# Optimization experiments

Hardware: AMD Instinct MI355X
Metric: run time of the kernel (lower is better)

## Reference

```python
import jax, jax.numpy as jnp
import numpy as np

PS, PAD, STRIDE = 3, 1, 1  # patch_size, padding, strides


def _unfold(x, ps, pad, stride):
    # torch F.unfold: [N, C, H, W] -> [N, C*ps*ps, L], channel-major (c, i, j) ordering
    N, C, H, Wd = x.shape
    xp = jnp.pad(x, ((0, 0), (0, 0), (pad, pad), (pad, pad)))
    Ho = (H + 2 * pad - ps) // stride + 1
    Wo = (Wd + 2 * pad - ps) // stride + 1
    cols = [xp[:, :, i:i + stride * Ho:stride, j:j + stride * Wo:stride]
            for i in range(ps) for j in range(ps)]  # ps*ps tensors of [N, C, Ho, Wo]
    cols = jnp.stack(cols, axis=2)                  # [N, C, ps*ps, Ho, Wo]
    return cols.reshape(N, C * ps * ps, Ho * Wo)


def _fold(cols, out_hw, ps, pad, stride):
    # torch F.fold (scatter-add inverse of unfold)
    N, CPP, L = cols.shape
    C = CPP // (ps * ps)
    H, Wd = out_hw
    Ho = (H + 2 * pad - ps) // stride + 1
    Wo = (Wd + 2 * pad - ps) // stride + 1
    cols = cols.reshape(N, C, ps, ps, Ho, Wo)
    out = jnp.zeros((N, C, H + 2 * pad, Wd + 2 * pad), cols.dtype)
    for i in range(ps):
        for j in range(ps):
            out = out.at[:, :, i:i + stride * Ho:stride, j:j + stride * Wo:stride].add(cols[:, :, i, j])
    return out[:, :, pad:pad + H, pad:pad + Wd]


def _l2norm(x, eps=1e-12):
    n = jnp.sqrt(jnp.sum(x * x, axis=-1, keepdims=True))
    return x / jnp.maximum(n, eps)


def setup_inputs() -> dict:
    key = jax.random.key(0)
    k1, k2, k3, k4 = jax.random.split(key, 4)
    shp = (2, 64, 5, 5, 48, 48)  # b, c, ah, aw, h, w
    return {
        "x1": jax.random.normal(k1, shp, dtype=jnp.float32),
        "x2": jax.random.normal(k2, shp, dtype=jnp.float32),
        "x3": jax.random.normal(k3, shp, dtype=jnp.float32),
        "W": jax.random.normal(k4, (8, 64), dtype=jnp.float32) * 0.05,  # 1x1 conv, c -> c//8
    }


def reference(x1, x2, x3, W):
    b, c, ah, aw, h, w = x1.shape
    A = ah * aw

    def flat(x):  # b c ah aw h w -> (b ah aw) c h w
        return x.transpose(0, 2, 3, 1, 4, 5).reshape(b * A, c, h, w)

    q = jnp.einsum('oc,nchw->nohw', W, flat(x1))  # 1x1 conv, no bias
    k = jnp.einsum('oc,nchw->nohw', W, flat(x2))
    v = flat(x3)

    qc = _unfold(q, PS, PAD, STRIDE)  # [(b ah aw), p_q, L]
    kc = _unfold(k, PS, PAD, STRIDE)
    vc = _unfold(v, PS, PAD, STRIDE)  # [(b ah aw), p_v, L]
    L = vc.shape[-1]
    p_v = vc.shape[1]

    def re(t):  # (b ah aw) p n -> b n (ah aw p)
        p = t.shape[1]
        return t.reshape(b, A, p, L).transpose(0, 3, 1, 2).reshape(b, L, A * p)

    Q = _l2norm(re(qc))
    K = _l2norm(re(kc))
    V = re(vc)  # [b, L, A*p_v]

    attn = jnp.einsum('bnd,bmd->bnm', Q, K)       # [b, L, L] cosine similarity
    idx = jnp.argmax(attn, axis=-1)               # [b, L] hard attention
    out = jnp.take_along_axis(V, idx[:, :, None], axis=1)  # gather rows of V

    # b n (ah aw p) -> (b ah aw) p n
    out = out.reshape(b, L, A, p_v).transpose(0, 2, 3, 1).reshape(b * A, p_v, L)
    out = _fold(out, (h, w), PS, PAD, STRIDE)     # [(b ah aw), c, h, w]
    return out.reshape(b, ah, aw, c, h, w).transpose(0, 3, 1, 2, 4, 5)
```

## Files before the change

### kernel.cpp

```cpp
#include <hip/hip_runtime.h>
#include <math.h>
#include <float.h>

#define NPIX 2304
#define NPAD 2500
#define PLANE 573440
#define MARGIN 3e-4f

#define OFF_QP     0u
#define OFF_KP     1146880u
#define OFF_PLANES 2293760u
#define OFF_TAIL   4587520u
#define OFF_NK     4751360u
#define OFF_INVNK  4756360u
#define OFF_PVAL   4760968u
#define OFF_PSEC   4982152u
#define OFF_PIDX   5203336u
#define OFF_IDX    5424520u
#define OFF_S      5429128u
#define OFF_SOFF   OFF_S
#define SSTRIDE    6250000L
#define PLANE_SH   573440

typedef __attribute__((ext_vector_type(8))) short short8;
typedef __attribute__((ext_vector_type(4))) float f32x4;

__device__ __forceinline__ unsigned short bfhi(float f) {
    unsigned u = __float_as_uint(f);
    return (unsigned short)((u + 0x7FFFu + ((u >> 16) & 1u)) >> 16);
}

__device__ __forceinline__ void gload_lds16(const void* g, void* l) {
    __builtin_amdgcn_global_load_lds(
        (const __attribute__((address_space(1))) unsigned int*)g,
        (__attribute__((address_space(3))) unsigned int*)l, 16, 0, 0);
}

__global__ __launch_bounds__(256) void k_zero(float4* __restrict__ p, int n4) {
    int i = blockIdx.x * 256 + threadIdx.x;
    const int stride = gridDim.x * 256;
    const float4 z = { 0.f, 0.f, 0.f, 0.f };
    for (; i < n4; i += stride) p[i] = z;
}

__global__ __launch_bounds__(256) void k_qk(const float* __restrict__ x1,
                                            const float* __restrict__ x2,
                                            const float* __restrict__ W,
                                            float* __restrict__ qp,
                                            float* __restrict__ kp,
                                            unsigned short* __restrict__ planes,
                                            unsigned short* __restrict__ tail) {
    __shared__ float Ws[512];
    const int t = threadIdx.x;
    Ws[t] = W[t];
    Ws[t + 256] = W[t + 256];
    __syncthreads();
    const int img = blockIdx.x / 9;
    const int chunk = blockIdx.x % 9;
    const int pix = chunk * 256 + t;
    const int b = img / 25, a = img % 25;
    const int y = pix / 48, x = pix % 48;

    float q[8], k[8];
#pragma unroll
    for (int o = 0; o < 8; ++o) { q[o] = 0.f; k[o] = 0.f; }

    const float* p1 = x1 + (size_t)b * 64 * 57600 + a * 2304 + pix;
    const float* p2 = x2 + (size_t)b * 64 * 57600 + a * 2304 + pix;
#pragma unroll 8
    for (int c = 0; c < 64; ++c) {
        float v1 = p1[c * 57600];
        float v2 = p2[c * 57600];
#pragma unroll
        for (int o = 0; o < 8; ++o) {
            float w = Ws[o * 64 + c];
            q[o] = fmaf(w, v1, q[o]);
            k[o] = fmaf(w, v2, k[o]);
        }
    }
    const int p = (y + 1) * 50 + (x + 1);
    float* qd = qp + (size_t)b * PLANE + (size_t)p * 224 + a * 8;
    float* kd = kp + (size_t)b * PLANE + (size_t)p * 224 + a * 8;
    float4 q0 = { q[0], q[1], q[2], q[3] }, q1 = { q[4], q[5], q[6], q[7] };
    float4 k0 = { k[0], k[1], k[2], k[3] }, k1 = { k[4], k[5], k[6], k[7] };
    *(float4*)qd = q0; *(float4*)(qd + 4) = q1;
    *(float4*)kd = k0; *(float4*)(kd + 4) = k1;

    const int P = p >> 7, r = p & 127, cc = a >> 2, dq = a & 3;
    const int g = r * 4 + ((dq + (r >> 1)) & 3);
    const size_t goff = ((size_t)(P * 7 + cc) * 512 + g) * 8;
    short8 qh, ql, kh, kl;
#pragma unroll
    for (int o = 0; o < 8; ++o) {
        unsigned short h = bfhi(q[o]);
        qh[o] = (short)h;
        ql[o] = (short)bfhi(q[o] - __uint_as_float(((unsigned)h) << 16));
        h = bfhi(k[o]);
        kh[o] = (short)h;
        kl[o] = (short)bfhi(k[o] - __uint_as_float(((unsigned)h) << 16));
    }
    *(short8*)(planes + (size_t)(0 * 2 + b) * PLANE_SH + goff) = qh;
    *(short8*)(planes + (size_t)(1 * 2 + b) * PLANE_SH + goff) = ql;
    *(short8*)(planes + (size_t)(2 * 2 + b) * PLANE_SH + goff) = kh;
    *(short8*)(planes + (size_t)(3 * 2 + b) * PLANE_SH + goff) = kl;

    if (a == 24) {
        unsigned short* qt = tail + (((size_t)(0 * 2 + b) * 20 + P) << 12);
        unsigned short* kt = tail + (((size_t)(1 * 2 + b) * 20 + P) << 12);
        short8 zz = { 0, 0, 0, 0, 0, 0, 0, 0 };
#define GOF(qq) ((r * 4 + (((qq) + (r >> 1)) & 3)) * 8)
        *(short8*)(qt + GOF(0)) = qh;
        *(short8*)(qt + GOF(1)) = qh;
        *(short8*)(qt + GOF(2)) = ql;
        *(short8*)(qt + GOF(3)) = zz;
        *(short8*)(kt + GOF(0)) = kh;
        *(short8*)(kt + GOF(1)) = kl;
        *(short8*)(kt + GOF(2)) = kh;
        *(short8*)(kt + GOF(3)) = zz;
#undef GOF
    }
}

__global__ void k_nk(const float* __restrict__ kp, float* __restrict__ nk) {
    int t = blockIdx.x * 256 + threadIdx.x;
    if (t >= 2 * NPAD) return;
    int b = t / NPAD, p = t - b * NPAD;
    const float* src = kp + (size_t)b * PLANE + (size_t)p * 224;
    float s = 0.f;
    for (int d = 0; d < 200; d += 4) {
        float4 v = *(const float4*)(src + d);
        s = fmaf(v.x, v.x, s); s = fmaf(v.y, v.y, s);
        s = fmaf(v.z, v.z, s); s = fmaf(v.w, v.w, s);
    }
    nk[t] = s;
}

__global__ void k_invnk(const float* __restrict__ nk, float* __restrict__ invNk) {
    int t = blockIdx.x * 256 + threadIdx.x;
    if (t >= 2 * NPIX) return;
    int b = t / NPIX, m = t - b * NPIX;
    int my = m / 48, mx = m % 48;
    const float* nb = nk + b * NPAD;
    float s = 0.f;
#pragma unroll
    for (int i = 0; i < 3; ++i)
#pragma unroll
        for (int j = 0; j < 3; ++j)
            s += nb[(my + i) * 50 + mx + j];
    invNk[t] = 1.0f / fmaxf(sqrtf(s), 1e-12f);
}

__global__ __launch_bounds__(256, 2) void k_mfma2(const unsigned short* __restrict__ planes,
                                                  const unsigned short* __restrict__ tail,
                                                  float* __restrict__ S,
                                                  long sStride, int bofs) {
    __shared__ unsigned short Abuf[2][4096];
    __shared__ unsigned short Bbuf[2][4096];
    const int t = threadIdx.x;
    const int nwg = gridDim.x * gridDim.y * gridDim.z;
    const int lin = (blockIdx.z * gridDim.y + blockIdx.y) * gridDim.x + blockIdx.x;
    const int work = (lin & 7) * (nwg >> 3) + (lin >> 3);
    const int z = work / 400;
    const int rem = work - z * 400;
    const int wy = rem / 20, wx = rem - (rem / 20) * 20;
    const int b = bofs + z;

    const unsigned short* Ahi = planes + (size_t)(0 * 2 + b) * PLANE_SH;
    const unsigned short* Alo = planes + (size_t)(1 * 2 + b) * PLANE_SH;
    const unsigned short* Bhi = planes + (size_t)(2 * 2 + b) * PLANE_SH;
    const unsigned short* Blo = planes + (size_t)(3 * 2 + b) * PLANE_SH;
    float* Sb = S + (size_t)z * sStride;

    const int p0 = wy * 128, r0 = wx * 128;
    const int wid = t >> 6, l = t & 63;
    const int lp = l & 15, dq = l >> 4;
    const int wqp = (wid >> 1) * 64, wqr = (wid & 1) * 64;

    int aoff[4], boff[4];
#pragma unroll
    for (int tr = 0; tr < 4; ++tr) {
        int rA = wqp + tr * 16 + lp;
        aoff[tr] = (rA * 4 + ((dq + (rA >> 1)) & 3)) * 8;
        int rB = wqr + tr * 16 + lp;
        boff[tr] = (rB * 4 + ((dq + (rB >> 1)) & 3)) * 8;
    }

    f32x4 acc[4][4];
#pragma unroll
    for (int i = 0; i < 4; ++i)
#pragma unroll
        for (int j = 0; j < 4; ++j) acc[i][j] = (f32x4){0.f, 0.f, 0.f, 0.f};

#define STAGE(buf, ks)                                                          \
    {                                                                           \
        const unsigned short *gA, *gB;                                          \
        if ((ks) < 18) {                                                        \
            const int term = (ks) / 6, c = (ks) - term * 6;                     \
            gA = (term < 2 ? Ahi : Alo) + ((size_t)(wy * 7 + c) << 12);         \
            gB = (term != 1 ? Bhi : Blo) + ((size_t)(wx * 7 + c) << 12);        \
        } else {                                                                \
            gA = tail + (((size_t)(0 * 2 + b) * 20 + wy) << 12);                \
            gB = tail + (((size_t)(1 * 2 + b) * 20 + wx) << 12);                \
        }                                                                       \
        unsigned short* lA = &Abuf[buf][wid * 512];                             \
        unsigned short* lB = &Bbuf[buf][wid * 512];                             \
        gload_lds16(gA + t * 8, lA);                                            \
        gload_lds16(gA + 2048 + t * 8, lA + 2048);                              \
        gload_lds16(gB + t * 8, lB);                                            \
        gload_lds16(gB + 2048 + t * 8, lB + 2048);                              \
    }

    STAGE(0, 0);
    asm volatile("s_waitcnt vmcnt(0)" ::: "memory");
    __syncthreads();

    int cur = 0;
    for (int ks = 0; ks < 19; ++ks) {
        if (ks + 1 < 19) STAGE(cur ^ 1, ks + 1);
        {
            const unsigned short* Ab = &Abuf[cur][0];
            const unsigned short* Bb = &Bbuf[cur][0];
            short8 af[4], bfr[4];
#pragma unroll
            for (int tr = 0; tr < 4; ++tr) af[tr] = *(const short8*)(Ab + aoff[tr]);
#pragma unroll
            for (int tc = 0; tc < 4; ++tc) bfr[tc] = *(const short8*)(Bb + boff[tc]);
#pragma unroll
            for (int tr = 0; tr < 4; ++tr)
#pragma unroll
                for (int tc = 0; tc < 4; ++tc)
                    acc[tr][tc] = __builtin_amdgcn_mfma_f32_16x16x32_bf16(
                        af[tr], bfr[tc], acc[tr][tc], 0, 0, 0);
        }
        if (ks + 1 < 19) {
            asm volatile("s_waitcnt vmcnt(0)" ::: "memory");
            __syncthreads();
            cur ^= 1;
        }
    }
#undef STAGE

#pragma unroll
    for (int tr = 0; tr < 4; ++tr) {
#pragma unroll
        for (int v = 0; v < 4; ++v) {
            const int p = p0 + wqp + tr * 16 + dq * 4 + v;
            if (p < NPAD) {
                float* srow_ = Sb + (size_t)p * NPAD;
#pragma unroll
                for (int tc = 0; tc < 4; ++tc) {
                    const int c = r0 + wqr + tc * 16 + lp;
                    if (c < NPAD) srow_[c] = acc[tr][tc][v];
                }
            }
        }
    }
}

__global__ __launch_bounds__(384) void k_argmax(const float* __restrict__ S,
                                                const float* __restrict__ invNk,
                                                float* __restrict__ pval,
                                                float* __restrict__ psec,
                                                int* __restrict__ pidx,
                                                long sStride, int bofs) {
    __shared__ float band[3][50][50];
    const int t = threadIdx.x;
    const int nwg = gridDim.x * gridDim.y * gridDim.z;
    const int lin = (blockIdx.z * gridDim.y + blockIdx.y) * gridDim.x + blockIdx.x;
    const int work = (lin & 7) * (nwg >> 3) + (lin >> 3);
    const int z = work / 2304;
    const int w2 = work - z * 2304;
    const int ly = w2 / 48;
    const int my = w2 - ly * 48;
    const int batch = bofs + z;
    const float* Sb = S + (size_t)z * sStride;

    {
        const int rt = t >> 3, ct = t & 7;
        for (int rr = rt; rr < 150; rr += 48) {
            const int i = (rr >= 100) ? 2 : (rr >= 50 ? 1 : 0);
            const int uu = rr - i * 50;
            const float* srow = Sb + (size_t)((ly + i) * 50 + uu) * NPAD + (my + i) * 50;
            float* drow = &band[i][uu][0];
            *(float2*)(drow + 2 * ct)      = *(const float2*)(srow + 2 * ct);
            *(float2*)(drow + 16 + 2 * ct) = *(const float2*)(srow + 16 + 2 * ct);
            *(float2*)(drow + 32 + 2 * ct) = *(const float2*)(srow + 32 + 2 * ct);
            if (ct == 0) *(float2*)(drow + 48) = *(const float2*)(srow + 48);
        }
    }
    __syncthreads();

    const int lx = t >> 3;
    const int mc = t & 7;
    const float* inb = invNk + batch * NPIX;
    const float* bp = &band[0][lx][mc];

    float b1 = -FLT_MAX, b2 = -FLT_MAX;
    int i1 = 0x7FFFFFFF;

#pragma unroll
    for (int k = 0; k < 6; ++k) {
        const float* p = bp + 8 * k;
        float s = p[0]    + p[51]   + p[102]
                + p[2500] + p[2551] + p[2602]
                + p[5000] + p[5051] + p[5102];
        int m = my * 48 + mc + (k << 3);
        float v = s * inb[m];
        if (v > b1 || (v == b1 && m < i1)) { b2 = b1; b1 = v; i1 = m; }
        else b2 = fmaxf(b2, v);
    }
#pragma unroll
    for (int off = 1; off < 8; off <<= 1) {
        float ob1 = __shfl_xor(b1, off, 64);
        int oi1 = __shfl_xor(i1, off, 64);
        float ob2 = __shfl_xor(b2, off, 64);
        if (ob1 > b1 || (ob1 == b1 && oi1 < i1)) { b2 = fmaxf(b1, ob2); b1 = ob1; i1 = oi1; }
        else b2 = fmaxf(b2, ob1);
    }
    if (mc == 0) {
        int o = (batch * 48 + my) * NPIX + ly * 48 + lx;
        pval[o] = b1;
        psec[o] = b2;
        pidx[o] = i1;
    }
}

__global__ __launch_bounds__(256) void k_sel(const float* __restrict__ qp,
                                             const float* __restrict__ kp,
                                             const float* __restrict__ S,
                                             const float* __restrict__ invNk,
                                             const float* __restrict__ pval,
                                             const float* __restrict__ psec,
                                             const int* __restrict__ pidx,
                                             int* __restrict__ idx,
                                             long sStride, int bofs) {
    const int t = threadIdx.x;
    const int lane = t & 63;
    const int row = blockIdx.x * 4 + (t >> 6);
    const int z = blockIdx.y;
    const int b = bofs + z;

    float v1 = -FLT_MAX, v2 = -FLT_MAX;
    int ii = 0x7FFFFFFF;
    if (lane < 48) {
        int o = (b * 48 + lane) * NPIX + row;
        v1 = pval[o];
        v2 = psec[o];
        ii = pidx[o];
    }
    float r1 = v1, r2 = v2;
    int ri = ii;
#pragma unroll
    for (int off = 1; off < 64; off <<= 1) {
        float o1 = __shfl_xor(r1, off, 64);
        int oi = __shfl_xor(ri, off, 64);
        float o2 = __shfl_xor(r2, off, 64);
        if (o1 > r1 || (o1 == r1 && oi < ri)) { r2 = fmaxf(o2, r1); r1 = o1; ri = oi; }
        else r2 = fmaxf(r2, o1);
    }
    if (lane == 0) idx[b * NPIX + row] = ri;
    if (r1 - r2 >= MARGIN) return;

    const float* Sb = S + (size_t)z * sStride;
    const float* Ap = qp + (size_t)b * PLANE;
    const float* Bp = kp + (size_t)b * PLANE;
    const float* inb = invNk + b * NPIX;
    const int ly = row / 48, lx = row % 48;
    const float th = r1 - MARGIN;

    unsigned long long mask = __ballot(lane < 48 && (v1 >= th || v2 >= th));
    float eb = -FLT_MAX;
    int ebi = 0x7FFFFFFF;
    while (mask) {
        const int my = __ffsll((long long)mask) - 1;
        mask &= mask - 1;
        float va = -FLT_MAX;
        if (lane < 48) {
            float s = 0.f;
#pragma unroll
            for (int i = 0; i < 3; ++i)
#pragma unroll
                for (int j = 0; j < 3; ++j)
                    s += Sb[(size_t)((ly + i) * 50 + lx + j) * NPAD + (my + i) * 50 + lane + j];
            va = s * inb[my * 48 + lane];
        }
        unsigned long long m2 = __ballot(lane < 48 && va >= th);
        while (m2) {
            const int mx = __ffsll((long long)m2) - 1;
            m2 &= m2 - 1;
            const int m = my * 48 + mx;
            float part = 0.f;
#pragma unroll
            for (int ij = 0; ij < 9; ++ij) {
                const float* qr = Ap + (size_t)((ly + ij / 3) * 50 + lx + ij % 3) * 224;
                const float* kr = Bp + (size_t)((my + ij / 3) * 50 + mx + ij % 3) * 224;
                for (int d = lane; d < 200; d += 64)
                    part = fmaf(qr[d], kr[d], part);
            }
#pragma unroll
            for (int off = 1; off < 64; off <<= 1)
                part += __shfl_xor(part, off, 64);
            const float v = part * inb[m];
            if (v > eb) { eb = v; ebi = m; }
        }
    }
    if (lane == 0 && ebi != 0x7FFFFFFF) idx[b * NPIX + row] = ebi;
}

__global__ void k_soff(const int* __restrict__ idx, int* __restrict__ soff) {
    int t = blockIdx.x * 256 + threadIdx.x;
    if (t >= 2 * NPIX) return;
    int b = t / NPIX, pix = t - b * NPIX;
    int y = pix / 48, x = pix % 48;
#pragma unroll
    for (int i = 0; i < 3; ++i) {
#pragma unroll
        for (int j = 0; j < 3; ++j) {
            int u = i * 3 + j;
            int yq = y + 1 - i, xq = x + 1 - j;
            int so = -1;
            if (yq >= 0 && yq < 48 && xq >= 0 && xq < 48) {
                int m = idx[b * NPIX + yq * 48 + xq];
                int my = m / 48, mx = m % 48;
                int yy = my + i - 1, xx = mx + j - 1;
                if (yy >= 0 && yy < 48 && xx >= 0 && xx < 48) so = yy * 48 + xx;
            }
            soff[(b * 9 + u) * NPIX + pix] = so;
        }
    }
}

#define CPB 4
__global__ __launch_bounds__(256) void k_out2(const float* __restrict__ x3,
                                              const int* __restrict__ soff,
                                              float* __restrict__ out) {
    __shared__ __align__(16) float plane[NPIX];
    const int t = threadIdx.x;
    const int img = blockIdx.x;
    const int b = img / 25, a = img % 25;

    int po[9][9];
#pragma unroll
    for (int u = 0; u < 9; ++u) {
        const int* sb = soff + (b * 9 + u) * NPIX;
#pragma unroll
        for (int k = 0; k < 9; ++k)
            po[k][u] = sb[k * 256 + t];
    }

    const size_t pbase = (size_t)b * 64 * 57600 + (size_t)a * 2304 +
                         (size_t)(blockIdx.y * CPB) * 57600;
    const float* gsrc = x3 + pbase;
    float* gdst = out + pbase;

    float4 r0, r1, r2;
    {
        const float4* g = (const float4*)gsrc;
        r0 = g[t]; r1 = g[t + 256];
        if (t < 64) r2 = g[t + 512];
    }
    float4* pl4 = (float4*)plane;
    pl4[t] = r0; pl4[t + 256] = r1;
    if (t < 64) pl4[t + 512] = r2;
    __syncthreads();

    for (int c = 0; c < CPB; ++c) {
        if (c + 1 < CPB) {
            const float4* g = (const float4*)(gsrc + (size_t)(c + 1) * 57600);
            r0 = g[t]; r1 = g[t + 256];
            if (t < 64) r2 = g[t + 512];
        }
        float* dst = gdst + (size_t)c * 57600;
#pragma unroll
        for (int k = 0; k < 9; ++k) {
            float acc = 0.f;
#pragma unroll
            for (int u = 0; u < 9; ++u) {
                int off = po[k][u];
                int ao = off < 0 ? 0 : off;
                float v = plane[ao];
                acc += (off < 0) ? 0.f : v;
            }
            dst[k * 256 + t] = acc;
        }
        __syncthreads();
        if (c + 1 < CPB) {
            pl4[t] = r0; pl4[t + 256] = r1;
            if (t < 64) pl4[t + 512] = r2;
        }
        __syncthreads();
    }
}

extern "C" void kernel_launch(void* const* d_in, const int* in_sizes, int n_in,
                              void* d_out, int out_size, void* d_ws, size_t ws_size,
                              hipStream_t stream) {
    const float* x1 = (const float*)d_in[0];
    const float* x2 = (const float*)d_in[1];
    const float* x3 = (const float*)d_in[2];
    const float* W  = (const float*)d_in[3];
    float* ws = (float*)d_ws;

    float* qp    = ws + OFF_QP;
    float* kp    = ws + OFF_KP;
    unsigned short* planes = (unsigned short*)(ws + OFF_PLANES);
    unsigned short* tail   = (unsigned short*)(ws + OFF_TAIL);
    float* nk    = ws + OFF_NK;
    float* invNk = ws + OFF_INVNK;
    float* pval  = ws + OFF_PVAL;
    float* psec  = ws + OFF_PSEC;
    int*   pidx  = (int*)(ws + OFF_PIDX);
    int*   idx   = (int*)(ws + OFF_IDX);
    float* S     = ws + OFF_S;
    int*   soff  = (int*)(ws + OFF_SOFF);
    float* out   = (float*)d_out;

    const bool bigS = ws_size >= (size_t)(OFF_S + 2UL * (unsigned long)SSTRIDE) * 4UL;

    k_zero<<<2048, 256, 0, stream>>>((float4*)(ws + OFF_QP), (int)(OFF_NK / 4));

    k_qk<<<450, 256, 0, stream>>>(x1, x2, W, qp, kp, planes, tail);
    k_nk<<<(2 * NPAD + 255) / 256, 256, 0, stream>>>(kp, nk);
    k_invnk<<<(2 * NPIX + 255) / 256, 256, 0, stream>>>(nk, invNk);

    if (bigS) {
        k_mfma2<<<dim3(20, 20, 2), 256, 0, stream>>>(planes, tail, S, SSTRIDE, 0);
        k_argmax<<<dim3(48, 48, 2), 384, 0, stream>>>(S, invNk, pval, psec, pidx, SSTRIDE, 0);
        k_sel<<<dim3(576, 2), 256, 0, stream>>>(qp, kp, S, invNk, pval, psec, pidx,
                                                idx, SSTRIDE, 0);
    } else {
        for (int b = 0; b < 2; ++b) {
            k_mfma2<<<dim3(20, 20, 1), 256, 0, stream>>>(planes, tail, S, 0L, b);
            k_argmax<<<dim3(48, 48, 1), 384, 0, stream>>>(S, invNk, pval, psec, pidx, 0L, b);
            k_sel<<<dim3(576, 1), 256, 0, stream>>>(qp, kp, S, invNk, pval, psec, pidx,
                                                    idx, 0L, b);
        }
    }
    k_soff<<<(2 * NPIX + 255) / 256, 256, 0, stream>>>(idx, soff);
    k_out2<<<dim3(50, 16), 256, 0, stream>>>(x3, soff, out);
}
```

Before: 156.2 us.

## Triple-buffer LDS in MFMA similarity GEMM with partial vmcnt waits

Grows the shared-memory A/B staging buffers from two to three stages and prefetches two k-steps ahead. Each iteration waits with a partial vmcnt so only the oldest stage's loads must have landed, then issues the next stage right after the LDS fragment reads. The aim is to keep global-to-LDS traffic in flight during MFMA work instead of draining all loads every step. In exchange LDS use per block rises from 32KB to 48KB, which may limit occupancy, and the vmcnt counts must match the four loads issued per stage.

Result: faster. 151.2 us (-3.2%).

```diff
diff --git a/kernel.cpp b/kernel.cpp
--- a/kernel.cpp
+++ b/kernel.cpp
@@ -154,8 +154,8 @@
                                                   const unsigned short* __restrict__ tail,
                                                   float* __restrict__ S,
                                                   long sStride, int bofs) {
-    __shared__ unsigned short Abuf[2][4096];
-    __shared__ unsigned short Bbuf[2][4096];
+    __shared__ unsigned short Abuf[3][4096];
+    __shared__ unsigned short Bbuf[3][4096];
     const int t = threadIdx.x;
     const int nwg = gridDim.x * gridDim.y * gridDim.z;
     const int lin = (blockIdx.z * gridDim.y + blockIdx.y) * gridDim.x + blockIdx.x;
@@ -210,35 +210,48 @@
         gload_lds16(gB + 2048 + t * 8, lB + 2048);                              \
     }
 
+#define ITER_BODY(BI, DO_STAGE, KS3)                                            \
+    {                                                                           \
+        const unsigned short* Ab = &Abuf[BI][0];                                \
+        const unsigned short* Bb = &Bbuf[BI][0];                                \
+        short8 af[4], bfr[4];                                                   \
+        _Pragma("unroll")                                                       \
+        for (int tr = 0; tr < 4; ++tr) af[tr] = *(const short8*)(Ab + aoff[tr]);\
+        _Pragma("unroll")                                                       \
+        for (int tc = 0; tc < 4; ++tc) bfr[tc] = *(const short8*)(Bb + boff[tc]);\
+        asm volatile("s_waitcnt lgkmcnt(0)" ::: "memory");                      \
+        __builtin_amdgcn_s_barrier();                                           \
+        if (DO_STAGE) STAGE(BI, KS3);                                           \
+        _Pragma("unroll")                                                       \
+        for (int tr = 0; tr < 4; ++tr)                                          \
+            _Pragma("unroll")                                                   \
+            for (int tc = 0; tc < 4; ++tc)                                      \
+                acc[tr][tc] = __builtin_amdgcn_mfma_f32_16x16x32_bf16(          \
+                    af[tr], bfr[tc], acc[tr][tc], 0, 0, 0);                     \
+    }
+
     STAGE(0, 0);
-    asm volatile("s_waitcnt vmcnt(0)" ::: "memory");
-    __syncthreads();
-
-    int cur = 0;
-    for (int ks = 0; ks < 19; ++ks) {
-        if (ks + 1 < 19) STAGE(cur ^ 1, ks + 1);
-        {
-            const unsigned short* Ab = &Abuf[cur][0];
-            const unsigned short* Bb = &Bbuf[cur][0];
-            short8 af[4], bfr[4];
-#pragma unroll
-            for (int tr = 0; tr < 4; ++tr) af[tr] = *(const short8*)(Ab + aoff[tr]);
-#pragma unroll
-            for (int tc = 0; tc < 4; ++tc) bfr[tc] = *(const short8*)(Bb + boff[tc]);
-#pragma unroll
-            for (int tr = 0; tr < 4; ++tr)
-#pragma unroll
-                for (int tc = 0; tc < 4; ++tc)
-                    acc[tr][tc] = __builtin_amdgcn_mfma_f32_16x16x32_bf16(
-                        af[tr], bfr[tc], acc[tr][tc], 0, 0, 0);
-        }
-        if (ks + 1 < 19) {
-            asm volatile("s_waitcnt vmcnt(0)" ::: "memory");
-            __syncthreads();
-            cur ^= 1;
-        }
+    STAGE(1, 1);
+    STAGE(2, 2);
+
+    for (int ks = 0; ks < 17; ++ks) {
+        asm volatile("s_waitcnt vmcnt(8)" ::: "memory");
+        __builtin_amdgcn_s_barrier();
+        const int bi = ks - (ks / 3) * 3;
+        ITER_BODY(bi, ks + 3 < 19, ks + 3)
+    }
+    {
+        asm volatile("s_waitcnt vmcnt(4)" ::: "memory");
+        __builtin_amdgcn_s_barrier();
+        ITER_BODY(2, false, 0)
+    }
+    {
+        asm volatile("s_waitcnt vmcnt(0)" ::: "memory");
+        __builtin_amdgcn_s_barrier();
+        ITER_BODY(0, false, 0)
     }
 #undef STAGE
+#undef ITER_BODY
 
 #pragma unroll
     for (int tr = 0; tr < 4; ++tr) {
```
